# Kernel optimization log

Hardware: AMD Instinct MI355X
Metric: run time of the kernel (lower is better)

The kernel has to match this reference:

```python
import jax, jax.numpy as jnp
import numpy as np

BSZ, SEQ, T, ENC, HID = 32, 2048, 32, 512, 512


def setup_inputs() -> dict:
    key = jax.random.key(0)
    ks = jax.random.split(key, 8)
    L = SEQ // T  # uniform turn length -> end ids cover every token
    end_ids = jnp.broadcast_to((jnp.arange(T, dtype=jnp.int32) + 1) * L - 1, (BSZ, T))
    s = 1.0 / np.sqrt(HID)
    return {
        "encoder_output": jax.random.normal(ks[0], (BSZ, SEQ, ENC), jnp.float32),
        "end_ids": end_ids,
        "W_ih": jax.random.uniform(ks[1], (4 * HID, ENC), jnp.float32, -s, s),
        "W_hh": jax.random.uniform(ks[2], (4 * HID, HID), jnp.float32, -s, s),
        "b_ih": jax.random.uniform(ks[3], (4 * HID,), jnp.float32, -s, s),
        "b_hh": jax.random.uniform(ks[4], (4 * HID,), jnp.float32, -s, s),
        "fc_w": jax.random.uniform(ks[5], (1, HID + ENC), jnp.float32, -s, s),
        "fc_b": jnp.zeros((1,), jnp.float32),
    }


def reference(encoder_output, end_ids, W_ih, W_hh, b_ih, b_hh, fc_w, fc_b):
    bsz, S, E = encoder_output.shape
    Tn = end_ids.shape[1]
    H = W_hh.shape[1]

    # ---- ragged segment-mean pooling: token t in turn j iff prev_end < t <= end[j]
    tok = jnp.arange(S)
    seg = jax.vmap(lambda e: jnp.searchsorted(e, tok))(end_ids)  # [bsz,S]
    gid = (seg + jnp.arange(bsz)[:, None] * Tn).reshape(-1)
    sums = jax.ops.segment_sum(encoder_output.reshape(-1, E), gid, num_segments=bsz * Tn)
    starts = jnp.concatenate([jnp.zeros((bsz, 1), end_ids.dtype), end_ids[:, :-1] + 1], axis=1)
    counts = (end_ids - starts + 1).astype(encoder_output.dtype)  # [bsz,Tn]
    turn_states = sums.reshape(bsz, Tn, E) / counts[..., None]

    # ---- all sliding windows of 3 consecutive turns
    J = Tn - 3
    widx = jnp.arange(J)[:, None] + jnp.arange(3)[None, :]  # [J,3]
    src = turn_states[:, widx].reshape(bsz * J, 3, E)  # [N,3,E]

    # ---- single-layer LSTM (pytorch gate order i,f,g,o), take last hidden state
    bias = b_ih + b_hh

    def step(carry, x_t):
        h, c = carry
        g = x_t @ W_ih.T + h @ W_hh.T + bias
        i_, f_, g_, o_ = jnp.split(g, 4, axis=-1)
        c = jax.nn.sigmoid(f_) * c + jax.nn.sigmoid(i_) * jnp.tanh(g_)
        h = jax.nn.sigmoid(o_) * jnp.tanh(c)
        return (h, c), None

    h0 = jnp.zeros((bsz * J, H), src.dtype)
    (hT, _), _ = jax.lax.scan(step, (h0, h0), jnp.swapaxes(src, 0, 1))

    # ---- con_fc([src_last, tgt]) decomposes into src-part + tgt-part of the weight
    sscore = (hT @ fc_w[0, :H]).reshape(bsz, J)  # [bsz,J]
    tscore = turn_states @ fc_w[0, H:]  # [bsz,Tn]
    kidx = jnp.arange(J)[:, None] + 3 + jnp.arange(J)[None, :]  # [J,J] candidate turn ids
    valid = kidx < Tn
    kc = jnp.clip(kidx, 0, Tn - 1)
    logits = sscore[:, :, None] + tscore[:, kc] + fc_b[0]  # [bsz,J,J]
    logits = jnp.where(valid[None], logits, jnp.float32(-1e9))
    # cross entropy with target index 0 (the j+3 turn is the positive)
    loss = jax.nn.logsumexp(logits, axis=-1) - logits[..., 0]  # [bsz,J]
    return jnp.mean(loss)
```

## Files before the change

### kernel.cpp

```cpp
#include <hip/hip_runtime.h>
#include <math.h>

#define BSZ   32
#define SEQL  2048
#define TN    32
#define ENCD  512
#define HIDD  512
#define JW    29
#define NW    (BSZ * JW)

typedef short bf16x8 __attribute__((ext_vector_type(8)));
typedef float f32x4  __attribute__((ext_vector_type(4)));

__device__ __forceinline__ float sigm(float x) { return 1.f / (1.f + expf(-x)); }

__device__ __forceinline__ unsigned short f2bf(float x) {
    union { float f; unsigned u; } v; v.f = x;
    unsigned u = v.u;
    u += 0x7FFF + ((u >> 16) & 1);
    return (unsigned short)(u >> 16);
}
__device__ __forceinline__ float bf2f(short s) {
    union { unsigned u; float f; } v; v.u = ((unsigned)(unsigned short)s) << 16;
    return v.f;
}

#define GLOAD_LDS16(gp, lp)                                                    \
    __builtin_amdgcn_global_load_lds(                                          \
        (const __attribute__((address_space(1))) void*)(gp),                   \
        (__attribute__((address_space(3))) void*)(lp), 16, 0, 0)

__global__ __launch_bounds__(256) void prep_k(const float* __restrict__ enc,
                                              const int* __restrict__ end_ids,
                                              short* __restrict__ tsbf,
                                              const float* __restrict__ w1,
                                              const float* __restrict__ w2,
                                              short* __restrict__ o1,
                                              short* __restrict__ o2) {
    int tid = threadIdx.x;
    if (blockIdx.x >= 1024) {
        int idx = (blockIdx.x - 1024) * 256 + tid;
        int t = idx >> 17;
        int i = idx & 131071;
        const float* s = (t ? w2 : w1) + (size_t)i * 8;
        short* o = (t ? o2 : o1) + (size_t)i * 8;
        float4 a = ((const float4*)s)[0];
        float4 b = ((const float4*)s)[1];
        union { short v[8]; bf16x8 p; } r;
        r.v[0] = (short)f2bf(a.x); r.v[1] = (short)f2bf(a.y);
        r.v[2] = (short)f2bf(a.z); r.v[3] = (short)f2bf(a.w);
        r.v[4] = (short)f2bf(b.x); r.v[5] = (short)f2bf(b.y);
        r.v[6] = (short)f2bf(b.z); r.v[7] = (short)f2bf(b.w);
        *(bf16x8*)o = r.p;
        return;
    }
    int blk = blockIdx.x;
    int j = blk & 31;
    int b = blk >> 5;
    int e_end   = end_ids[blk];
    int e_start = j ? (end_ids[blk - 1] + 1) : 0;
    int col = (tid & 127) << 2;
    int tr  = tid >> 7;
    const float* base = enc + (size_t)b * SEQL * ENCD + col;
    float ax = 0.f, ay = 0.f, az = 0.f, aw = 0.f;
    for (int t = e_start + tr; t <= e_end; t += 2) {
        float4 v = *(const float4*)(base + (size_t)t * ENCD);
        ax += v.x; ay += v.y; az += v.z; aw += v.w;
    }
    __shared__ float4 part[128];
    if (tr) part[tid & 127] = make_float4(ax, ay, az, aw);
    __syncthreads();
    if (!tr) {
        float4 o = part[tid];
        float inv = 1.f / (float)(e_end - e_start + 1);
        union { unsigned short v[4]; uint2 p; } q;
        q.v[0] = f2bf((ax + o.x) * inv); q.v[1] = f2bf((ay + o.y) * inv);
        q.v[2] = f2bf((az + o.z) * inv); q.v[3] = f2bf((aw + o.w) * inv);
        *(uint2*)(tsbf + (size_t)blk * ENCD + col) = q.p;
    }
}

template <int STEP>
__global__ __launch_bounds__(256) void gemm_lstm(const short* __restrict__ A,
                                                 const short* __restrict__ B,
                                                 float* __restrict__ XW,
                                                 float* __restrict__ Cb,
                                                 short* __restrict__ Hout,
                                                 const float* __restrict__ b_ih,
                                                 const float* __restrict__ b_hh) {
    __shared__ short Als[2][8 * 512];
    __shared__ short Bls[2][16 * 512];
    int tid = threadIdx.x, w = tid >> 6, lane = tid & 63;
    int l15 = lane & 15, l4 = lane >> 4;
    int m0 = blockIdx.y * 64;
    int hcol0 = blockIdx.x * 32;
    int wm = (w >> 1) * 32, wh = (w & 1) * 16;
    const short* Aptr = A + (size_t)m0 * 512;
    f32x4 acc[2][4] = {};

    auto stage = [&](int sel, int k0) {
#pragma unroll
        for (int i = 0; i < 6; ++i) {
            int c = w * 6 + i;
            if (c < 8) {
                int unit = c * 64 + lane;
                int row = unit >> 3, slot = unit & 7;
                int scol = slot ^ (row & 7);
                GLOAD_LDS16(Aptr + (size_t)row * 512 + k0 + scol * 8,
                            &Als[sel][c * 512]);
            } else {
                int cc = c - 8;
                int unit = cc * 64 + lane;
                int rr = unit >> 3, slot = unit & 7;
                int grow = (rr >> 5) * 512 + hcol0 + (rr & 31);
                int scol = slot ^ (rr & 7);
                GLOAD_LDS16(B + (size_t)grow * 512 + k0 + scol * 8,
                            &Bls[sel][cc * 512]);
            }
        }
    };

    stage(0, 0);
    __syncthreads();
    int sel = 0;
    for (int t = 0; t < 8; ++t) {
        if (t < 7) stage(sel ^ 1, (t + 1) * 64);
        bf16x8 af[2][2], bfr[4][2];
#pragma unroll
        for (int kk = 0; kk < 2; ++kk) {
#pragma unroll
            for (int fm = 0; fm < 2; ++fm) {
                int row = wm + fm * 16 + l15;
                int s = (kk * 4 + l4) ^ (row & 7);
                af[fm][kk] = *(const bf16x8*)&Als[sel][row * 64 + s * 8];
            }
#pragma unroll
            for (int g = 0; g < 4; ++g) {
                int rr = g * 32 + wh + l15;
                int s = (kk * 4 + l4) ^ (rr & 7);
                bfr[g][kk] = *(const bf16x8*)&Bls[sel][rr * 64 + s * 8];
            }
        }
#pragma unroll
        for (int kk = 0; kk < 2; ++kk)
#pragma unroll
            for (int fm = 0; fm < 2; ++fm)
#pragma unroll
                for (int g = 0; g < 4; ++g)
                    acc[fm][g] = __builtin_amdgcn_mfma_f32_16x16x32_bf16(
                        af[fm][kk], bfr[g][kk], acc[fm][g], 0, 0, 0);
        __syncthreads();
        sel ^= 1;
    }

    int hcol = hcol0 + wh + l15;
    float b0 = 0.f, b1 = 0.f, b2 = 0.f, b3 = 0.f;
    if (STEP == 1) {
        b0 = b_ih[hcol]        + b_hh[hcol];
        b1 = b_ih[512 + hcol]  + b_hh[512 + hcol];
        b2 = b_ih[1024 + hcol] + b_hh[1024 + hcol];
        b3 = b_ih[1536 + hcol] + b_hh[1536 + hcol];
    }
#pragma unroll
    for (int fm = 0; fm < 2; ++fm) {
        int rbase = m0 + wm + fm * 16 + l4 * 4;
#pragma unroll
        for (int r = 0; r < 4; ++r) {
            int row = rbase + r;
            float gi = acc[fm][0][r], gf = acc[fm][1][r];
            float gg = acc[fm][2][r], go = acc[fm][3][r];
            float cn;
            if (STEP == 1) {
                gi += b0; gf += b1; gg += b2; go += b3;
                float* xp = XW + (size_t)row * 2048 + hcol;
                xp[0] = gi; xp[512] = gf; xp[1024] = gg; xp[1536] = go;
                cn = sigm(gi) * tanhf(gg);
            } else {
                int xr = row + (STEP - 1); if (xr > 1023) xr = 1023;
                const float* xp = XW + (size_t)xr * 2048 + hcol;
                gi += xp[0]; gf += xp[512]; gg += xp[1024]; go += xp[1536];
                float cprev = Cb[(size_t)row * 512 + hcol];
                cn = sigm(gf) * cprev + sigm(gi) * tanhf(gg);
            }
            float h = sigm(go) * tanhf(cn);
            if (STEP < 3) Cb[(size_t)row * 512 + hcol] = cn;
            Hout[(size_t)row * 512 + hcol] = (short)f2bf(h);
        }
    }
}

__global__ __launch_bounds__(256) void scores_k(const short* __restrict__ h3,
                                                const short* __restrict__ tsbf,
                                                const float* __restrict__ fcw,
                                                float* __restrict__ ss,
                                                float* __restrict__ tsc) {
    int row = blockIdx.x * 4 + (threadIdx.x >> 6);
    int lane = threadIdx.x & 63;
    if (row >= NW + BSZ * TN) return;
    const short* x;
    const float* wv;
    if (row < NW) {
        int turn = (row / JW) * TN + (row % JW);
        x = h3 + (size_t)turn * HIDD; wv = fcw;
    } else {
        x = tsbf + (size_t)(row - NW) * ENCD; wv = fcw + HIDD;
    }
    int k = lane << 3;
    bf16x8 xv = *(const bf16x8*)(x + k);
    float4 w0 = *(const float4*)(wv + k);
    float4 w1 = *(const float4*)(wv + k + 4);
    float acc = bf2f(xv[0]) * w0.x + bf2f(xv[1]) * w0.y +
                bf2f(xv[2]) * w0.z + bf2f(xv[3]) * w0.w +
                bf2f(xv[4]) * w1.x + bf2f(xv[5]) * w1.y +
                bf2f(xv[6]) * w1.z + bf2f(xv[7]) * w1.w;
#pragma unroll
    for (int s = 32; s; s >>= 1) acc += __shfl_down(acc, s, 64);
    if (lane == 0) {
        if (row < NW) ss[row] = acc;
        else tsc[row - NW] = acc;
    }
}

__global__ __launch_bounds__(1024) void loss_k(const float* __restrict__ ss,
                                               const float* __restrict__ tsc,
                                               const float* __restrict__ fcb,
                                               float* __restrict__ out) {
    int tid = threadIdx.x;
    float l = 0.f;
    if (tid < NW) {
        int b = tid / JW, j = tid % JW;
        float base = ss[tid] + fcb[0];
        int nv = JW - j;
        float l0 = 0.f, m = -1e30f;
        for (int k = 0; k < nv; ++k) {
            float lg = base + tsc[b * TN + j + 3 + k];
            if (k == 0) l0 = lg;
            m = fmaxf(m, lg);
        }
        float sum = 0.f;
        for (int k = 0; k < nv; ++k) {
            float lg = base + tsc[b * TN + j + 3 + k];
            sum += expf(lg - m);
        }
        l = (m + logf(sum)) - l0;
    }
    __shared__ float red[16];
#pragma unroll
    for (int s = 32; s; s >>= 1) l += __shfl_down(l, s, 64);
    int wid = tid >> 6, lane = tid & 63;
    if (lane == 0) red[wid] = l;
    __syncthreads();
    if (tid == 0) {
        float tot = 0.f;
        for (int i = 0; i < 16; ++i) tot += red[i];
        out[0] = tot / (float)NW;
    }
}

extern "C" void kernel_launch(void* const* d_in, const int* in_sizes, int n_in,
                              void* d_out, int out_size, void* d_ws, size_t ws_size,
                              hipStream_t stream) {
    const float* enc     = (const float*)d_in[0];
    const int*   end_ids = (const int*)d_in[1];
    const float* W_ih    = (const float*)d_in[2];
    const float* W_hh    = (const float*)d_in[3];
    const float* b_ih    = (const float*)d_in[4];
    const float* b_hh    = (const float*)d_in[5];
    const float* fc_w    = (const float*)d_in[6];
    const float* fc_b    = (const float*)d_in[7];
    float* out = (float*)d_out;

    float* ws = (float*)d_ws;
    float* XW  = ws;
    float* Cb  = XW + 1024 * 2048;
    float* ss  = Cb + 1024 * 512;
    float* tsc = ss + 1024;
    short* tsbf   = (short*)(tsc + 1024);
    short* Wih_bf = tsbf + 1024 * 512;
    short* Whh_bf = Wih_bf + 2048 * 512;
    short* HA     = Whh_bf + 2048 * 512;
    short* HB     = HA + 1024 * 512;

    prep_k<<<2048, 256, 0, stream>>>(enc, end_ids, tsbf, W_ih, W_hh, Wih_bf, Whh_bf);
    gemm_lstm<1><<<dim3(16, 16), 256, 0, stream>>>(tsbf, Wih_bf, XW, Cb, HA, b_ih, b_hh);
    gemm_lstm<2><<<dim3(16, 16), 256, 0, stream>>>(HA, Whh_bf, XW, Cb, HB, b_ih, b_hh);
    gemm_lstm<3><<<dim3(16, 16), 256, 0, stream>>>(HB, Whh_bf, XW, Cb, HA, b_ih, b_hh);
    scores_k<<<(NW + BSZ * TN + 3) / 4, 256, 0, stream>>>(HA, tsbf, fc_w, ss, tsc);
    loss_k<<<1, 1024, 0, stream>>>(ss, tsc, fc_b, out);
}
```

Before: 73.09 us.

## Fuse LSTM steps, scoring and loss into one persistent kernel with grid barriers

The three per-step GEMM+LSTM launches, the scores kernel and the loss kernel become a single persistent kernel of 256 blocks. The blocks synchronise through atomic grid barriers, keep the cell state and final hidden state in registers, and store the input projection XW in bf16 instead of fp32. Target-turn scores are now computed inside the pooling kernel, which also uses 512 threads with more loads in flight. This removes launch gaps and several global round trips. In exchange it relies on all 256 blocks being resident at once, and storing XW in bf16 adds rounding error.

```diff
diff --git a/kernel.cpp b/kernel.cpp
--- a/kernel.cpp
+++ b/kernel.cpp
@@ -8,6 +8,7 @@
 #define HIDD  512
 #define JW    29
 #define NW    (BSZ * JW)
+#define NBLK  256
 
 typedef short bf16x8 __attribute__((ext_vector_type(8)));
 typedef float f32x4  __attribute__((ext_vector_type(4)));
@@ -30,16 +31,21 @@
         (const __attribute__((address_space(1))) void*)(gp),                   \
         (__attribute__((address_space(3))) void*)(lp), 16, 0, 0)
 
-__global__ __launch_bounds__(256) void prep_k(const float* __restrict__ enc,
+__global__ __launch_bounds__(512) void prep_k(const float* __restrict__ enc,
                                               const int* __restrict__ end_ids,
                                               short* __restrict__ tsbf,
                                               const float* __restrict__ w1,
                                               const float* __restrict__ w2,
                                               short* __restrict__ o1,
-                                              short* __restrict__ o2) {
+                                              short* __restrict__ o2,
+                                              const float* __restrict__ fcw,
+                                              float* __restrict__ tsc,
+                                              unsigned* __restrict__ cnt) {
     int tid = threadIdx.x;
-    if (blockIdx.x >= 1024) {
-        int idx = (blockIdx.x - 1024) * 256 + tid;
+    int bid = blockIdx.x;
+    if (bid >= 1024) {
+        if (bid == 1024 && tid < 8) cnt[tid] = 0;
+        int idx = (bid - 1024) * 512 + tid;
         int t = idx >> 17;
         int i = idx & 131071;
         const float* s = (t ? w2 : w1) + (size_t)i * 8;
@@ -54,206 +60,236 @@
         *(bf16x8*)o = r.p;
         return;
     }
-    int blk = blockIdx.x;
-    int j = blk & 31;
-    int b = blk >> 5;
-    int e_end   = end_ids[blk];
-    int e_start = j ? (end_ids[blk - 1] + 1) : 0;
+    int j = bid & 31;
+    int b = bid >> 5;
+    int e_end   = end_ids[bid];
+    int e_start = j ? (end_ids[bid - 1] + 1) : 0;
     int col = (tid & 127) << 2;
     int tr  = tid >> 7;
     const float* base = enc + (size_t)b * SEQL * ENCD + col;
     float ax = 0.f, ay = 0.f, az = 0.f, aw = 0.f;
-    for (int t = e_start + tr; t <= e_end; t += 2) {
+    float bx = 0.f, by = 0.f, bz = 0.f, bw = 0.f;
+    for (int t = e_start + tr; t <= e_end; t += 8) {
         float4 v = *(const float4*)(base + (size_t)t * ENCD);
         ax += v.x; ay += v.y; az += v.z; aw += v.w;
-    }
-    __shared__ float4 part[128];
-    if (tr) part[tid & 127] = make_float4(ax, ay, az, aw);
+        int t2 = t + 4;
+        if (t2 <= e_end) {
+            float4 u = *(const float4*)(base + (size_t)t2 * ENCD);
+            bx += u.x; by += u.y; bz += u.z; bw += u.w;
+        }
+    }
+    ax += bx; ay += by; az += bz; aw += bw;
+    __shared__ float4 part[3][128];
+    __shared__ float red[128];
+    if (tr) part[tr - 1][tid & 127] = make_float4(ax, ay, az, aw);
     __syncthreads();
     if (!tr) {
-        float4 o = part[tid];
+        float4 p0 = part[0][tid], p1 = part[1][tid], p2 = part[2][tid];
         float inv = 1.f / (float)(e_end - e_start + 1);
+        float mx = (ax + p0.x + p1.x + p2.x) * inv;
+        float my = (ay + p0.y + p1.y + p2.y) * inv;
+        float mz = (az + p0.z + p1.z + p2.z) * inv;
+        float mw = (aw + p0.w + p1.w + p2.w) * inv;
         union { unsigned short v[4]; uint2 p; } q;
-        q.v[0] = f2bf((ax + o.x) * inv); q.v[1] = f2bf((ay + o.y) * inv);
-        q.v[2] = f2bf((az + o.z) * inv); q.v[3] = f2bf((aw + o.w) * inv);
-        *(uint2*)(tsbf + (size_t)blk * ENCD + col) = q.p;
-    }
-}
-
-template <int STEP>
-__global__ __launch_bounds__(256) void gemm_lstm(const short* __restrict__ A,
-                                                 const short* __restrict__ B,
-                                                 float* __restrict__ XW,
-                                                 float* __restrict__ Cb,
-                                                 short* __restrict__ Hout,
-                                                 const float* __restrict__ b_ih,
-                                                 const float* __restrict__ b_hh) {
+        q.v[0] = f2bf(mx); q.v[1] = f2bf(my); q.v[2] = f2bf(mz); q.v[3] = f2bf(mw);
+        *(uint2*)(tsbf + (size_t)bid * ENCD + col) = q.p;
+        float4 wv = *(const float4*)(fcw + HIDD + col);
+        red[tid] = mx * wv.x + my * wv.y + mz * wv.z + mw * wv.w;
+    }
+    __syncthreads();
+    if (tid < 64) {
+        float s = red[tid] + red[tid + 64];
+#pragma unroll
+        for (int sh = 32; sh; sh >>= 1) s += __shfl_down(s, sh, 64);
+        if (tid == 0) tsc[bid] = s;
+    }
+}
+
+__device__ __forceinline__ void gridbar(unsigned* cnt, int phase) {
+    __syncthreads();
+    if (threadIdx.x == 0) {
+        __threadfence();
+        __hip_atomic_fetch_add(&cnt[phase], 1u, __ATOMIC_RELEASE,
+                               __HIP_MEMORY_SCOPE_AGENT);
+        while (__hip_atomic_load(&cnt[phase], __ATOMIC_ACQUIRE,
+                                 __HIP_MEMORY_SCOPE_AGENT) < (unsigned)NBLK) {}
+        __threadfence();
+    }
+    __syncthreads();
+}
+
+__global__ __launch_bounds__(256) void mega_k(
+        const short* __restrict__ tsbf, const short* __restrict__ Wih,
+        const short* __restrict__ Whh, ushort4* __restrict__ XWq,
+        short* __restrict__ HA, short* __restrict__ HB,
+        float* __restrict__ ss_part, const float* __restrict__ tsc,
+        const float* __restrict__ b_ih, const float* __restrict__ b_hh,
+        const float* __restrict__ fcw, const float* __restrict__ fcb,
+        unsigned* __restrict__ cnt, float* __restrict__ out) {
     __shared__ short Als[2][8 * 512];
     __shared__ short Bls[2][16 * 512];
     int tid = threadIdx.x, w = tid >> 6, lane = tid & 63;
     int l15 = lane & 15, l4 = lane >> 4;
-    int m0 = blockIdx.y * 64;
-    int hcol0 = blockIdx.x * 32;
+    int bx = blockIdx.x & 15, by = blockIdx.x >> 4;
+    int m0 = by * 64, hcol0 = bx * 32;
     int wm = (w >> 1) * 32, wh = (w & 1) * 16;
-    const short* Aptr = A + (size_t)m0 * 512;
-    f32x4 acc[2][4] = {};
-
-    auto stage = [&](int sel, int k0) {
-#pragma unroll
-        for (int i = 0; i < 6; ++i) {
-            int c = w * 6 + i;
-            if (c < 8) {
-                int unit = c * 64 + lane;
-                int row = unit >> 3, slot = unit & 7;
-                int scol = slot ^ (row & 7);
-                GLOAD_LDS16(Aptr + (size_t)row * 512 + k0 + scol * 8,
-                            &Als[sel][c * 512]);
-            } else {
-                int cc = c - 8;
-                int unit = cc * 64 + lane;
-                int rr = unit >> 3, slot = unit & 7;
-                int grow = (rr >> 5) * 512 + hcol0 + (rr & 31);
-                int scol = slot ^ (rr & 7);
-                GLOAD_LDS16(B + (size_t)grow * 512 + k0 + scol * 8,
-                            &Bls[sel][cc * 512]);
+    int hcol = hcol0 + wh + l15;
+    float bb0 = b_ih[hcol]        + b_hh[hcol];
+    float bb1 = b_ih[512 + hcol]  + b_hh[512 + hcol];
+    float bb2 = b_ih[1024 + hcol] + b_hh[1024 + hcol];
+    float bb3 = b_ih[1536 + hcol] + b_hh[1536 + hcol];
+    float cc[2][4];
+    float hreg[2][4];
+
+    for (int step = 1; step <= 3; ++step) {
+        const short* A = (step == 1) ? tsbf : (step == 2 ? HA : HB);
+        const short* B = (step == 1) ? Wih : Whh;
+        const short* Aptr = A + (size_t)m0 * 512;
+        f32x4 acc[2][4] = {};
+
+        auto stage = [&](int sel, int k0) {
+#pragma unroll
+            for (int i = 0; i < 6; ++i) {
+                int c = w * 6 + i;
+                if (c < 8) {
+                    int unit = c * 64 + lane;
+                    int row = unit >> 3, slot = unit & 7;
+                    int scol = slot ^ (row & 7);
+                    GLOAD_LDS16(Aptr + (size_t)row * 512 + k0 + scol * 8,
+                                &Als[sel][c * 512]);
+                } else {
+                    int ccn = c - 8;
+                    int unit = ccn * 64 + lane;
+                    int rr = unit >> 3, slot = unit & 7;
+                    int grow = (rr >> 5) * 512 + hcol0 + (rr & 31);
+                    int scol = slot ^ (rr & 7);
+                    GLOAD_LDS16(B + (size_t)grow * 512 + k0 + scol * 8,
+                                &Bls[sel][ccn * 512]);
+                }
             }
-        }
-    };
-
-    stage(0, 0);
-    __syncthreads();
-    int sel = 0;
-    for (int t = 0; t < 8; ++t) {
-        if (t < 7) stage(sel ^ 1, (t + 1) * 64);
-        bf16x8 af[2][2], bfr[4][2];
-#pragma unroll
-        for (int kk = 0; kk < 2; ++kk) {
-#pragma unroll
-            for (int fm = 0; fm < 2; ++fm) {
-                int row = wm + fm * 16 + l15;
-                int s = (kk * 4 + l4) ^ (row & 7);
-                af[fm][kk] = *(const bf16x8*)&Als[sel][row * 64 + s * 8];
+        };
+
+        stage(0, 0);
+        __syncthreads();
+        int sel = 0;
+        for (int t = 0; t < 8; ++t) {
+            if (t < 7) stage(sel ^ 1, (t + 1) * 64);
+            bf16x8 af[2][2], bfr[4][2];
+#pragma unroll
+            for (int kk = 0; kk < 2; ++kk) {
+#pragma unroll
+                for (int fm = 0; fm < 2; ++fm) {
+                    int row = wm + fm * 16 + l15;
+                    int s = (kk * 4 + l4) ^ (row & 7);
+                    af[fm][kk] = *(const bf16x8*)&Als[sel][row * 64 + s * 8];
+                }
+#pragma unroll
+                for (int g = 0; g < 4; ++g) {
+                    int rr = g * 32 + wh + l15;
+                    int s = (kk * 4 + l4) ^ (rr & 7);
+                    bfr[g][kk] = *(const bf16x8*)&Bls[sel][rr * 64 + s * 8];
+                }
             }
 #pragma unroll
-            for (int g = 0; g < 4; ++g) {
-                int rr = g * 32 + wh + l15;
-                int s = (kk * 4 + l4) ^ (rr & 7);
-                bfr[g][kk] = *(const bf16x8*)&Bls[sel][rr * 64 + s * 8];
+            for (int kk = 0; kk < 2; ++kk)
+#pragma unroll
+                for (int fm = 0; fm < 2; ++fm)
+#pragma unroll
+                    for (int g = 0; g < 4; ++g)
+                        acc[fm][g] = __builtin_amdgcn_mfma_f32_16x16x32_bf16(
+                            af[fm][kk], bfr[g][kk], acc[fm][g], 0, 0, 0);
+            __syncthreads();
+            sel ^= 1;
+        }
+
+#pragma unroll
+        for (int fm = 0; fm < 2; ++fm) {
+            int rbase = m0 + wm + fm * 16 + l4 * 4;
+#pragma unroll
+            for (int r = 0; r < 4; ++r) {
+                int row = rbase + r;
+                float gi = acc[fm][0][r], gf = acc[fm][1][r];
+                float gg = acc[fm][2][r], go = acc[fm][3][r];
+                float cn;
+                if (step == 1) {
+                    gi += bb0; gf += bb1; gg += bb2; go += bb3;
+                    ushort4 q;
+                    q.x = f2bf(gi); q.y = f2bf(gf); q.z = f2bf(gg); q.w = f2bf(go);
+                    XWq[(size_t)row * 512 + hcol] = q;
+                    cn = sigm(gi) * tanhf(gg);
+                } else {
+                    int xr = row + (step - 1); if (xr > 1023) xr = 1023;
+                    ushort4 q = XWq[(size_t)xr * 512 + hcol];
+                    gi += bf2f((short)q.x); gf += bf2f((short)q.y);
+                    gg += bf2f((short)q.z); go += bf2f((short)q.w);
+                    cn = sigm(gf) * cc[fm][r] + sigm(gi) * tanhf(gg);
+                }
+                cc[fm][r] = cn;
+                float h = sigm(go) * tanhf(cn);
+                if (step == 1)      HA[(size_t)row * 512 + hcol] = (short)f2bf(h);
+                else if (step == 2) HB[(size_t)row * 512 + hcol] = (short)f2bf(h);
+                else                hreg[fm][r] = h;
             }
         }
-#pragma unroll
-        for (int kk = 0; kk < 2; ++kk)
-#pragma unroll
-            for (int fm = 0; fm < 2; ++fm)
-#pragma unroll
-                for (int g = 0; g < 4; ++g)
-                    acc[fm][g] = __builtin_amdgcn_mfma_f32_16x16x32_bf16(
-                        af[fm][kk], bfr[g][kk], acc[fm][g], 0, 0, 0);
+        if (step < 3) gridbar(cnt, step - 1);
+    }
+
+    float fcv = fcw[hcol];
+    float* sred = (float*)&Als[0][0];
+    float vals[2][4];
+#pragma unroll
+    for (int fm = 0; fm < 2; ++fm)
+#pragma unroll
+        for (int r = 0; r < 4; ++r) {
+            float v = hreg[fm][r] * fcv;
+#pragma unroll
+            for (int m = 1; m < 16; m <<= 1) v += __shfl_xor(v, m, 64);
+            vals[fm][r] = v;
+        }
+    if ((w & 1) == 0 && l15 == 0)
+#pragma unroll
+        for (int fm = 0; fm < 2; ++fm)
+#pragma unroll
+            for (int r = 0; r < 4; ++r) sred[wm + fm * 16 + l4 * 4 + r] = vals[fm][r];
+    __syncthreads();
+    if ((w & 1) == 1 && l15 == 0)
+#pragma unroll
+        for (int fm = 0; fm < 2; ++fm)
+#pragma unroll
+            for (int r = 0; r < 4; ++r) sred[wm + fm * 16 + l4 * 4 + r] += vals[fm][r];
+    __syncthreads();
+    if (tid < 64) ss_part[(size_t)(m0 + tid) * 16 + bx] = sred[tid];
+
+    gridbar(cnt, 2);
+
+    if (blockIdx.x == 0) {
+        float l = 0.f;
+        for (int n = tid; n < NW; n += 256) {
+            int b = n / JW, j = n - b * JW;
+            int turn = b * TN + j;
+            const float* sp = ss_part + (size_t)turn * 16;
+            float s = 0.f;
+#pragma unroll
+            for (int k2 = 0; k2 < 16; ++k2) s += sp[k2];
+            float base2 = s + fcb[0];
+            int nv = JW - j;
+            const float* tp = tsc + b * TN + j + 3;
+            float m = -1e30f, l0 = 0.f;
+            for (int k2 = 0; k2 < nv; ++k2) {
+                float lg = base2 + tp[k2];
+                if (k2 == 0) l0 = lg;
+                m = fmaxf(m, lg);
+            }
+            float sum = 0.f;
+            for (int k2 = 0; k2 < nv; ++k2) sum += expf(base2 + tp[k2] - m);
+            l += (m + logf(sum)) - l0;
+        }
+#pragma unroll
+        for (int sh = 32; sh; sh >>= 1) l += __shfl_down(l, sh, 64);
+        float* red2 = (float*)&Bls[0][0];
+        if (lane == 0) red2[w] = l;
         __syncthreads();
-        sel ^= 1;
-    }
-
-    int hcol = hcol0 + wh + l15;
-    float b0 = 0.f, b1 = 0.f, b2 = 0.f, b3 = 0.f;
-    if (STEP == 1) {
-        b0 = b_ih[hcol]        + b_hh[hcol];
-        b1 = b_ih[512 + hcol]  + b_hh[512 + hcol];
-        b2 = b_ih[1024 + hcol] + b_hh[1024 + hcol];
-        b3 = b_ih[1536 + hcol] + b_hh[1536 + hcol];
-    }
-#pragma unroll
-    for (int fm = 0; fm < 2; ++fm) {
-        int rbase = m0 + wm + fm * 16 + l4 * 4;
-#pragma unroll
-        for (int r = 0; r < 4; ++r) {
-            int row = rbase + r;
-            float gi = acc[fm][0][r], gf = acc[fm][1][r];
-            float gg = acc[fm][2][r], go = acc[fm][3][r];
-            float cn;
-            if (STEP == 1) {
-                gi += b0; gf += b1; gg += b2; go += b3;
-                float* xp = XW + (size_t)row * 2048 + hcol;
-                xp[0] = gi; xp[512] = gf; xp[1024] = gg; xp[1536] = go;
-                cn = sigm(gi) * tanhf(gg);
-            } else {
-                int xr = row + (STEP - 1); if (xr > 1023) xr = 1023;
-                const float* xp = XW + (size_t)xr * 2048 + hcol;
-                gi += xp[0]; gf += xp[512]; gg += xp[1024]; go += xp[1536];
-                float cprev = Cb[(size_t)row * 512 + hcol];
-                cn = sigm(gf) * cprev + sigm(gi) * tanhf(gg);
-            }
-            float h = sigm(go) * tanhf(cn);
-            if (STEP < 3) Cb[(size_t)row * 512 + hcol] = cn;
-            Hout[(size_t)row * 512 + hcol] = (short)f2bf(h);
-        }
-    }
-}
-
-__global__ __launch_bounds__(256) void scores_k(const short* __restrict__ h3,
-                                                const short* __restrict__ tsbf,
-                                                const float* __restrict__ fcw,
-                                                float* __restrict__ ss,
-                                                float* __restrict__ tsc) {
-    int row = blockIdx.x * 4 + (threadIdx.x >> 6);
-    int lane = threadIdx.x & 63;
-    if (row >= NW + BSZ * TN) return;
-    const short* x;
-    const float* wv;
-    if (row < NW) {
-        int turn = (row / JW) * TN + (row % JW);
-        x = h3 + (size_t)turn * HIDD; wv = fcw;
-    } else {
-        x = tsbf + (size_t)(row - NW) * ENCD; wv = fcw + HIDD;
-    }
-    int k = lane << 3;
-    bf16x8 xv = *(const bf16x8*)(x + k);
-    float4 w0 = *(const float4*)(wv + k);
-    float4 w1 = *(const float4*)(wv + k + 4);
-    float acc = bf2f(xv[0]) * w0.x + bf2f(xv[1]) * w0.y +
-                bf2f(xv[2]) * w0.z + bf2f(xv[3]) * w0.w +
-                bf2f(xv[4]) * w1.x + bf2f(xv[5]) * w1.y +
-                bf2f(xv[6]) * w1.z + bf2f(xv[7]) * w1.w;
-#pragma unroll
-    for (int s = 32; s; s >>= 1) acc += __shfl_down(acc, s, 64);
-    if (lane == 0) {
-        if (row < NW) ss[row] = acc;
-        else tsc[row - NW] = acc;
-    }
-}
-
-__global__ __launch_bounds__(1024) void loss_k(const float* __restrict__ ss,
-                                               const float* __restrict__ tsc,
-                                               const float* __restrict__ fcb,
-                                               float* __restrict__ out) {
-    int tid = threadIdx.x;
-    float l = 0.f;
-    if (tid < NW) {
-        int b = tid / JW, j = tid % JW;
-        float base = ss[tid] + fcb[0];
-        int nv = JW - j;
-        float l0 = 0.f, m = -1e30f;
-        for (int k = 0; k < nv; ++k) {
-            float lg = base + tsc[b * TN + j + 3 + k];
-            if (k == 0) l0 = lg;
-            m = fmaxf(m, lg);
-        }
-        float sum = 0.f;
-        for (int k = 0; k < nv; ++k) {
-            float lg = base + tsc[b * TN + j + 3 + k];
-            sum += expf(lg - m);
-        }
-        l = (m + logf(sum)) - l0;
-    }
-    __shared__ float red[16];
-#pragma unroll
-    for (int s = 32; s; s >>= 1) l += __shfl_down(l, s, 64);
-    int wid = tid >> 6, lane = tid & 63;
-    if (lane == 0) red[wid] = l;
-    __syncthreads();
-    if (tid == 0) {
-        float tot = 0.f;
-        for (int i = 0; i < 16; ++i) tot += red[i];
-        out[0] = tot / (float)NW;
+        if (tid == 0) out[0] = (red2[0] + red2[1] + red2[2] + red2[3]) / (float)NW;
     }
 }
 
@@ -270,21 +306,19 @@
     const float* fc_b    = (const float*)d_in[7];
     float* out = (float*)d_out;
 
-    float* ws = (float*)d_ws;
-    float* XW  = ws;
-    float* Cb  = XW + 1024 * 2048;
-    float* ss  = Cb + 1024 * 512;
-    float* tsc = ss + 1024;
-    short* tsbf   = (short*)(tsc + 1024);
+    short* tsbf   = (short*)d_ws;
     short* Wih_bf = tsbf + 1024 * 512;
     short* Whh_bf = Wih_bf + 2048 * 512;
     short* HA     = Whh_bf + 2048 * 512;
     short* HB     = HA + 1024 * 512;
-
-    prep_k<<<2048, 256, 0, stream>>>(enc, end_ids, tsbf, W_ih, W_hh, Wih_bf, Whh_bf);
-    gemm_lstm<1><<<dim3(16, 16), 256, 0, stream>>>(tsbf, Wih_bf, XW, Cb, HA, b_ih, b_hh);
-    gemm_lstm<2><<<dim3(16, 16), 256, 0, stream>>>(HA, Whh_bf, XW, Cb, HB, b_ih, b_hh);
-    gemm_lstm<3><<<dim3(16, 16), 256, 0, stream>>>(HB, Whh_bf, XW, Cb, HA, b_ih, b_hh);
-    scores_k<<<(NW + BSZ * TN + 3) / 4, 256, 0, stream>>>(HA, tsbf, fc_w, ss, tsc);
-    loss_k<<<1, 1024, 0, stream>>>(ss, tsc, fc_b, out);
-}
+    ushort4* XWq  = (ushort4*)(HB + 1024 * 512);
+    float* ss_part = (float*)(XWq + 1024 * 512);
+    float* tsc    = ss_part + 1024 * 16;
+    unsigned* cnt = (unsigned*)(tsc + 1024);
+
+    prep_k<<<1536, 512, 0, stream>>>(enc, end_ids, tsbf, W_ih, W_hh,
+                                     Wih_bf, Whh_bf, fc_w, tsc, cnt);
+    mega_k<<<NBLK, 256, 0, stream>>>(tsbf, Wih_bf, Whh_bf, XWq, HA, HB,
+                                     ss_part, tsc, b_ih, b_hh, fc_w, fc_b,
+                                     cnt, out);
+}
```

New measurement: 148.3 us. 2.03x slower.
